# Performance work log

Hardware: AMD Instinct MI355X
Metric: run time of the kernel (lower is better)

## Reference

```python
import jax, jax.numpy as jnp
import numpy as np

N_NODES = 100000
N_EDGES = 1600000
HIDDEN = 128
N_GRAPHS = 64
N_CLASSES = 10


def setup_inputs() -> dict:
    key = jax.random.key(0)
    ks = jax.random.split(key, 10)
    x = jax.random.normal(ks[0], (N_NODES, 1), dtype=jnp.float32)
    edge_index = jax.random.randint(ks[1], (2, N_EDGES), 0, N_NODES, dtype=jnp.int32)
    batch = jnp.sort(jax.random.randint(ks[2], (N_NODES,), 0, N_GRAPHS, dtype=jnp.int32))
    def glorot(k, shape):
        fan_in, fan_out = shape
        s = jnp.sqrt(6.0 / (fan_in + fan_out))
        return jax.random.uniform(k, shape, jnp.float32, -s, s)
    return {
        "x": x,
        "edge_index": edge_index,
        "batch": batch,
        "W1l": glorot(ks[3], (1, HIDDEN)),
        "W1r": glorot(ks[4], (1, HIDDEN)),
        "b1": jnp.zeros((HIDDEN,), jnp.float32),
        "W2l": glorot(ks[5], (HIDDEN, HIDDEN)),
        "W2r": glorot(ks[6], (HIDDEN, HIDDEN)),
        "b2": jnp.zeros((HIDDEN,), jnp.float32),
        "W3l": glorot(ks[7], (HIDDEN, HIDDEN)),
        "W3r": glorot(ks[8], (HIDDEN, HIDDEN)),
        "b3": jnp.zeros((HIDDEN,), jnp.float32),
        "Wfc": glorot(ks[9], (HIDDEN, N_CLASSES)),
        "bfc": jnp.zeros((N_CLASSES,), jnp.float32),
    }


def _sage_conv(x, src, dst, Wl, Wr, b, n_nodes):
    # mean aggregation of source features at destination nodes
    msg = x[src]                                              # [E, d_in]
    agg = jax.ops.segment_sum(msg, dst, num_segments=n_nodes)  # [N, d_in]
    cnt = jax.ops.segment_sum(jnp.ones((src.shape[0], 1), x.dtype), dst,
                              num_segments=n_nodes)            # [N, 1]
    mean = agg / jnp.maximum(cnt, 1.0)
    # PyG SAGEConv: lin_l(mean neighbors) + bias + lin_r(self)
    return mean @ Wl + b + x @ Wr


def reference(x, edge_index, batch, W1l, W1r, b1, W2l, W2r, b2,
              W3l, W3r, b3, Wfc, bfc):
    src, dst = edge_index[0], edge_index[1]
    n = x.shape[0]
    h = jax.nn.relu(_sage_conv(x, src, dst, W1l, W1r, b1, n))
    h = jax.nn.relu(_sage_conv(h, src, dst, W2l, W2r, b2, n))
    h = jax.nn.relu(_sage_conv(h, src, dst, W3l, W3r, b3, n))
    # global_mean_pool over graph ids in `batch`
    pooled = jax.ops.segment_sum(h, batch, num_segments=N_GRAPHS)
    gcnt = jax.ops.segment_sum(jnp.ones((n, 1), h.dtype), batch,
                               num_segments=N_GRAPHS)
    pooled = pooled / jnp.maximum(gcnt, 1.0)
    logits = pooled @ Wfc + bfc
    return jax.nn.log_softmax(logits, axis=1)
```

## Files before the change

### kernel.cpp

```cpp
#include <hip/hip_runtime.h>

typedef unsigned int u32;
typedef unsigned short u16;
typedef short bf16x8 __attribute__((ext_vector_type(8)));
typedef float f32x4 __attribute__((ext_vector_type(4)));
typedef float f32x2 __attribute__((ext_vector_type(2)));
typedef u32 u32x4 __attribute__((ext_vector_type(4)));

#define HBLK 256

__device__ __forceinline__ u16 f2bf(float f) {
  u32 u = __float_as_uint(f);
  u = (u + 0x7FFFu + ((u >> 16) & 1u)) >> 16;
  return (u16)u;
}
__device__ __forceinline__ float bf2f(u32 h) { return __uint_as_float(h << 16); }

__global__ void hist_wprep_kernel(const int* __restrict__ dst, int* __restrict__ boff,
                                  int* __restrict__ btotal, int E, int nbuk, int chunk,
                                  const float* __restrict__ W2l, const float* __restrict__ W2r,
                                  const float* __restrict__ W3l, const float* __restrict__ W3r,
                                  u16* __restrict__ wt2, u16* __restrict__ wt3,
                                  float* __restrict__ pooled, int* __restrict__ gcnt) {
  int idx = blockIdx.x * 256 + threadIdx.x;
  {
    int which = idx >> 15, r = idx & 32767;
    int j = r >> 8, k = r & 255;
    if (which == 0) {
      float v = (k < 128) ? W2l[k * 128 + j] : W2r[(k - 128) * 128 + j];
      wt2[r] = f2bf(v);
    } else {
      float v = (k < 128) ? W3l[k * 128 + j] : W3r[(k - 128) * 128 + j];
      wt3[r] = f2bf(v);
    }
    if (idx < 8192) pooled[idx] = 0.f;
    if (idx < 64) gcnt[idx] = 0;
  }
  __shared__ int h[1024];
  for (int i = threadIdx.x; i < nbuk; i += 256) h[i] = 0;
  __syncthreads();
  int b0 = blockIdx.x * chunk, b1 = min(b0 + chunk, E);
  for (int e = b0 + threadIdx.x; e < b1; e += 256)
    atomicAdd(&h[dst[e] >> 7], 1);
  __syncthreads();
  for (int i = threadIdx.x; i < nbuk; i += 256)
    boff[i * HBLK + blockIdx.x] = atomicAdd(&btotal[i], h[i]);
}

__global__ void scatter2_kernel(const int* __restrict__ src, const int* __restrict__ dst,
                                const int* __restrict__ btotal, const int* __restrict__ boff,
                                u32* __restrict__ part, int* __restrict__ bbase,
                                int E, int nbuk, int chunk) {
  __shared__ int bt[1024];
  __shared__ int wsum[256];
  __shared__ int cur[1024];
  int tid = threadIdx.x;
  int t4 = tid * 4;
  int v0 = (t4 + 0 < nbuk) ? btotal[t4 + 0] : 0;
  int v1 = (t4 + 1 < nbuk) ? btotal[t4 + 1] : 0;
  int v2 = (t4 + 2 < nbuk) ? btotal[t4 + 2] : 0;
  int v3 = (t4 + 3 < nbuk) ? btotal[t4 + 3] : 0;
  int sum = v0 + v1 + v2 + v3;
  wsum[tid] = sum;
  __syncthreads();
  for (int off = 1; off < 256; off <<= 1) {
    int t = (tid >= off) ? wsum[tid - off] : 0;
    __syncthreads();
    wsum[tid] += t;
    __syncthreads();
  }
  int excl = wsum[tid] - sum;
  bt[t4 + 0] = excl;
  bt[t4 + 1] = excl + v0;
  bt[t4 + 2] = excl + v0 + v1;
  bt[t4 + 3] = excl + v0 + v1 + v2;
  __syncthreads();
  for (int i = tid; i < nbuk; i += 256) {
    cur[i] = bt[i] + boff[i * HBLK + blockIdx.x];
    if (blockIdx.x == 0) bbase[i] = bt[i];
  }
  __syncthreads();
  int b0 = blockIdx.x * chunk, b1 = min(b0 + chunk, E);
  for (int e = b0 + tid; e < b1; e += 256) {
    int d = dst[e];
    int pos = atomicAdd(&cur[d >> 7], 1);
    part[pos] = (u32)src[e] | ((u32)(d & 127) << 25);
  }
}

__global__ void scatter3_kernel(const u32* __restrict__ part, const int* __restrict__ bbase,
                                const float* __restrict__ x,
                                const float* __restrict__ W1l, const float* __restrict__ W1r,
                                const float* __restrict__ b1,
                                int* __restrict__ roff, int* __restrict__ csr,
                                u32* __restrict__ h1, int E, int nbuk, int n) {
  int b = blockIdx.x;
  int tid = threadIdx.x;
  int base = bbase[b];
  int end = (b + 1 < nbuk) ? bbase[b + 1] : E;
  __shared__ int cnt[128];
  __shared__ int s[128];
  __shared__ int cur[128];
  __shared__ float xsum[128];
  __shared__ float meanv[128];
  __shared__ float wlA[128], wrA[128], bA[128];
  if (tid < 128) {
    cnt[tid] = 0; xsum[tid] = 0.f;
    wlA[tid] = W1l[tid]; wrA[tid] = W1r[tid]; bA[tid] = b1[tid];
  }
  __syncthreads();
  for (int e = base + tid; e < end; e += 256)
    atomicAdd(&cnt[part[e] >> 25], 1);
  __syncthreads();
  if (tid < 128) s[tid] = cnt[tid];
  __syncthreads();
  for (int off = 1; off < 128; off <<= 1) {
    int t = (tid >= off && tid < 128) ? s[tid - off] : 0;
    __syncthreads();
    if (tid < 128) s[tid] += t;
    __syncthreads();
  }
  if (tid < 128) {
    int excl = s[tid] - cnt[tid];
    cur[tid] = base + excl;
    int node = b * 128 + tid;
    if (node < n) roff[node] = base + excl;
  }
  if (b == 0 && tid == 0) roff[n] = E;
  __syncthreads();
  for (int e = base + tid; e < end; e += 256) {
    u32 p = part[e];
    int sidx = (int)(p & 0x1FFFFFFu);
    int pos = atomicAdd(&cur[p >> 25], 1);
    csr[pos] = sidx;
    atomicAdd(&xsum[p >> 25], x[sidx]);
  }
  __syncthreads();
  if (tid < 128) meanv[tid] = xsum[tid] / (float)max(cnt[tid], 1);
  __syncthreads();
  int nlocal = min(128, n - b * 128);
  for (int q = tid; q < nlocal * 64; q += 256) {
    int ln = q >> 6, w = q & 63;
    int node = b * 128 + ln;
    int j0 = w * 2;
    float m = meanv[ln], xs = x[node];
    float v0 = fmaxf(m * wlA[j0] + xs * wrA[j0] + bA[j0], 0.f);
    float v1 = fmaxf(m * wlA[j0 + 1] + xs * wrA[j0 + 1] + bA[j0 + 1], 0.f);
    h1[(size_t)node * 64 + w] = (u32)f2bf(v0) | ((u32)f2bf(v1) << 16);
  }
}

__global__ void agg_kernel(const int* __restrict__ csr, const int* __restrict__ roff,
                           const u32* __restrict__ hin, u32* __restrict__ outv, int n) {
  int wave = threadIdx.x >> 6, lane = threadIdx.x & 63;
  int i = blockIdx.x * 4 + wave;
  if (i >= n) return;
  int grp = lane >> 4, li = lane & 15;
  int e0 = roff[i], e1 = roff[i + 1];
  f32x2 a[4] = {};
  int e = e0 + grp;
  for (; e + 12 < e1; e += 16) {
    int s0 = csr[e], s1 = csr[e + 4], s2 = csr[e + 8], s3 = csr[e + 12];
    u32x4 v0 = *(const u32x4*)(hin + (size_t)s0 * 64 + li * 4);
    u32x4 v1 = *(const u32x4*)(hin + (size_t)s1 * 64 + li * 4);
    u32x4 v2 = *(const u32x4*)(hin + (size_t)s2 * 64 + li * 4);
    u32x4 v3 = *(const u32x4*)(hin + (size_t)s3 * 64 + li * 4);
#pragma unroll
    for (int w = 0; w < 4; ++w) {
      a[w] += (f32x2){bf2f(v0[w] & 0xFFFFu), bf2f(v0[w] >> 16)};
      a[w] += (f32x2){bf2f(v1[w] & 0xFFFFu), bf2f(v1[w] >> 16)};
      a[w] += (f32x2){bf2f(v2[w] & 0xFFFFu), bf2f(v2[w] >> 16)};
      a[w] += (f32x2){bf2f(v3[w] & 0xFFFFu), bf2f(v3[w] >> 16)};
    }
  }
  for (; e + 4 < e1; e += 8) {
    int s0 = csr[e], s1 = csr[e + 4];
    u32x4 v0 = *(const u32x4*)(hin + (size_t)s0 * 64 + li * 4);
    u32x4 v1 = *(const u32x4*)(hin + (size_t)s1 * 64 + li * 4);
#pragma unroll
    for (int w = 0; w < 4; ++w) {
      a[w] += (f32x2){bf2f(v0[w] & 0xFFFFu), bf2f(v0[w] >> 16)};
      a[w] += (f32x2){bf2f(v1[w] & 0xFFFFu), bf2f(v1[w] >> 16)};
    }
  }
  if (e < e1) {
    int s0 = csr[e];
    u32x4 v0 = *(const u32x4*)(hin + (size_t)s0 * 64 + li * 4);
#pragma unroll
    for (int w = 0; w < 4; ++w)
      a[w] += (f32x2){bf2f(v0[w] & 0xFFFFu), bf2f(v0[w] >> 16)};
  }
#pragma unroll
  for (int w = 0; w < 4; ++w) {
    a[w].x += __shfl_xor(a[w].x, 16, 64);
    a[w].y += __shfl_xor(a[w].y, 16, 64);
    a[w].x += __shfl_xor(a[w].x, 32, 64);
    a[w].y += __shfl_xor(a[w].y, 32, 64);
  }
  if (grp == 0) {
    float inv = 1.f / (float)max(e1 - e0, 1);
    u32x4 o;
#pragma unroll
    for (int w = 0; w < 4; ++w)
      o[w] = (u32)f2bf(a[w].x * inv) | ((u32)f2bf(a[w].y * inv) << 16);
    *(u32x4*)(outv + (size_t)i * 64 + li * 4) = o;
  }
}

__launch_bounds__(1024)
__global__ void mm_kernel(const u16* Aleft, const u16* Aright,
                          const u16* __restrict__ Wt, const float* __restrict__ bias,
                          u16* Out, int n) {
  __shared__ u16 wlds[16384];
  int wave = threadIdx.x >> 6;
  int lane = threadIdx.x & 63;
  int quad = lane >> 4, l16 = lane & 15;
  int row0 = blockIdx.x * 256 + wave * 16;
  int m = row0 + l16;
  int mc = m < n ? m : (n - 1);
  f32x4 acc[8] = {};
  const u16* Ah[2] = {Aleft, Aright};
#pragma unroll
  for (int phase = 0; phase < 2; ++phase) {
    if (phase) __syncthreads();
    for (int c = threadIdx.x; c < 2048; c += 1024) {
      int j = c >> 4, ch = c & 15;
      int swz = ch ^ (j & 15);
      *(u32x4*)(&wlds[j * 128 + swz * 8]) =
          *(const u32x4*)(&Wt[j * 256 + (phase * 16 + ch) * 8]);
    }
    __syncthreads();
    const u16* A = Ah[phase] + (size_t)mc * 128;
#pragma unroll
    for (int s = 0; s < 4; ++s) {
      bf16x8 a = *(const bf16x8*)(A + s * 32 + quad * 8);
      int cc = (s << 2) + quad;
      int swz = cc ^ l16;
#pragma unroll
      for (int t = 0; t < 8; ++t) {
        int j = t * 16 + l16;
        bf16x8 b = *(const bf16x8*)(&wlds[j * 128 + swz * 8]);
        acc[t] = __builtin_amdgcn_mfma_f32_16x16x32_bf16(a, b, acc[t], 0, 0, 0);
      }
    }
  }
#pragma unroll
  for (int t = 0; t < 8; ++t) {
    int j = t * 16 + l16;
    float bj = bias[j];
#pragma unroll
    for (int r = 0; r < 4; ++r) {
      int mr = row0 + quad * 4 + r;
      if (mr < n) {
        float v = acc[t][r] + bj;
        Out[(size_t)mr * 128 + j] = f2bf(fmaxf(v, 0.f));
      }
    }
  }
}

#define PB_NODES 128
__global__ void pool_partial(const int* __restrict__ batch, const u32* __restrict__ h3,
                             float* __restrict__ pooled, int* __restrict__ gcnt, int n) {
  __shared__ int bg[PB_NODES];
  int tid = threadIdx.x;
  int start = blockIdx.x * PB_NODES;
  int cntN = min(PB_NODES, n - start);
  if (tid < cntN) bg[tid] = batch[start + tid];
  __syncthreads();
  int wave = tid >> 6, lane = tid & 63;
  float a0 = 0.f, a1 = 0.f;
  int gcur = -1, cnt = 0;
  int k = wave;
  for (; k + 12 < cntN; k += 16) {
    u32 v0 = h3[(size_t)(start + k) * 64 + lane];
    u32 v1 = h3[(size_t)(start + k + 4) * 64 + lane];
    u32 v2 = h3[(size_t)(start + k + 8) * 64 + lane];
    u32 v3 = h3[(size_t)(start + k + 12) * 64 + lane];
    int g0 = bg[k], g1 = bg[k + 4], g2 = bg[k + 8], g3 = bg[k + 12];
    u32 vv[4] = {v0, v1, v2, v3};
    int gg[4] = {g0, g1, g2, g3};
#pragma unroll
    for (int q = 0; q < 4; ++q) {
      if (gg[q] != gcur) {
        if (gcur >= 0) {
          atomicAdd(&pooled[gcur * 128 + lane * 2], a0);
          atomicAdd(&pooled[gcur * 128 + lane * 2 + 1], a1);
          if (lane == 0) atomicAdd(&gcnt[gcur], cnt);
        }
        gcur = gg[q]; a0 = 0.f; a1 = 0.f; cnt = 0;
      }
      a0 += bf2f(vv[q] & 0xFFFFu);
      a1 += bf2f(vv[q] >> 16);
      cnt++;
    }
  }
  for (; k < cntN; k += 4) {
    u32 v = h3[(size_t)(start + k) * 64 + lane];
    int g = bg[k];
    if (g != gcur) {
      if (gcur >= 0) {
        atomicAdd(&pooled[gcur * 128 + lane * 2], a0);
        atomicAdd(&pooled[gcur * 128 + lane * 2 + 1], a1);
        if (lane == 0) atomicAdd(&gcnt[gcur], cnt);
      }
      gcur = g; a0 = 0.f; a1 = 0.f; cnt = 0;
    }
    a0 += bf2f(v & 0xFFFFu);
    a1 += bf2f(v >> 16);
    cnt++;
  }
  if (gcur >= 0) {
    atomicAdd(&pooled[gcur * 128 + lane * 2], a0);
    atomicAdd(&pooled[gcur * 128 + lane * 2 + 1], a1);
    if (lane == 0) atomicAdd(&gcnt[gcur], cnt);
  }
}

__global__ void head_kernel(const float* __restrict__ pooled, const int* __restrict__ gcnt,
                            const float* __restrict__ Wfc, const float* __restrict__ bfc,
                            float* __restrict__ out) {
  __shared__ float lg[64][10];
  int t = threadIdx.x;
  if (t < 640) {
    int g = t / 10, c = t % 10;
    float inv = 1.f / (float)max(gcnt[g], 1);
    float acc = bfc[c];
    for (int k = 0; k < 128; ++k) acc += pooled[g * 128 + k] * inv * Wfc[k * 10 + c];
    lg[g][c] = acc;
  }
  __syncthreads();
  if (t < 640) {
    int g = t / 10, c = t % 10;
    float mx = -1e30f;
    for (int q = 0; q < 10; ++q) mx = fmaxf(mx, lg[g][q]);
    float se = 0.f;
    for (int q = 0; q < 10; ++q) se += expf(lg[g][q] - mx);
    out[g * 10 + c] = lg[g][c] - mx - logf(se);
  }
}

extern "C" void kernel_launch(void* const* d_in, const int* in_sizes, int n_in,
                              void* d_out, int out_size, void* d_ws, size_t ws_size,
                              hipStream_t stream) {
  const float* x   = (const float*)d_in[0];
  const int* ei    = (const int*)d_in[1];
  const int* batch = (const int*)d_in[2];
  const float* W1l = (const float*)d_in[3];
  const float* W1r = (const float*)d_in[4];
  const float* b1  = (const float*)d_in[5];
  const float* W2l = (const float*)d_in[6];
  const float* W2r = (const float*)d_in[7];
  const float* b2  = (const float*)d_in[8];
  const float* W3l = (const float*)d_in[9];
  const float* W3r = (const float*)d_in[10];
  const float* b3  = (const float*)d_in[11];
  const float* Wfc = (const float*)d_in[12];
  const float* bfc = (const float*)d_in[13];
  float* out = (float*)d_out;
  int N = in_sizes[0];
  int E = in_sizes[1] / 2;
  const int* src = ei;
  const int* dst = ei + E;

  char* p = (char*)d_ws;
  auto alloc = [&](size_t bytes) { void* r = (void*)p; p += (bytes + 255) & ~(size_t)255; return r; };
  int* roff   = (int*)alloc((size_t)(N + 1) * 4);
  int* csr    = (int*)alloc((size_t)E * 4);
  u32* bufA   = (u32*)alloc((size_t)N * 64 * 4);
  u32* bufB   = (u32*)alloc((size_t)N * 64 * 4);
  u16* wt2    = (u16*)alloc(32768 * 2);
  u16* wt3    = (u16*)alloc(32768 * 2);
  float* pooled = (float*)alloc(64 * 128 * 4);
  int* gcnt   = (int*)alloc(64 * 4);
  int* btotal = (int*)alloc(1024 * 4);
  int* bbase  = (int*)alloc(1024 * 4);

  int nbuk = (N + 127) >> 7;
  int* boff = (int*)bufA;
  u32* part = (u32*)bufB;
  int chunk = (E + HBLK - 1) / HBLK;

  hipMemsetAsync(btotal, 0, 1024 * 4, stream);
  hist_wprep_kernel<<<HBLK, 256, 0, stream>>>(dst, boff, btotal, E, nbuk, chunk,
                                              W2l, W2r, W3l, W3r, wt2, wt3,
                                              pooled, gcnt);
  scatter2_kernel<<<HBLK, 256, 0, stream>>>(src, dst, btotal, boff, part, bbase,
                                            E, nbuk, chunk);
  scatter3_kernel<<<nbuk, 256, 0, stream>>>(part, bbase, x, W1l, W1r, b1,
                                            roff, csr, bufA, E, nbuk, N);
  agg_kernel<<<(N + 3) / 4, 256, 0, stream>>>(csr, roff, bufA, bufB, N);
  mm_kernel<<<(N + 255) / 256, 1024, 0, stream>>>((const u16*)bufB, (const u16*)bufA, wt2, b2,
                                                  (u16*)bufB, N);
  agg_kernel<<<(N + 3) / 4, 256, 0, stream>>>(csr, roff, bufB, bufA, N);
  mm_kernel<<<(N + 255) / 256, 1024, 0, stream>>>((const u16*)bufA, (const u16*)bufB, wt3, b3,
                                                  (u16*)bufA, N);
  pool_partial<<<(N + PB_NODES - 1) / PB_NODES, 256, 0, stream>>>(batch, bufA, pooled, gcnt, N);
  head_kernel<<<1, 640, 0, stream>>>(pooled, gcnt, Wfc, bfc, out);
}
```

Measured before the change: 349.3 us.

## Fuse neighbor mean aggregation with SAGE linear layers into one kernel

```diff
diff --git a/kernel.cpp b/kernel.cpp
--- a/kernel.cpp
+++ b/kernel.cpp
@@ -150,14 +150,27 @@
   }
 }
 
-__global__ void agg_kernel(const int* __restrict__ csr, const int* __restrict__ roff,
-                           const u32* __restrict__ hin, u32* __restrict__ outv, int n) {
+__launch_bounds__(1024)
+__global__ void aggmm_kernel(const int* __restrict__ csr, const int* __restrict__ roff,
+                             const u32* __restrict__ hin, const u16* __restrict__ Wt,
+                             const float* __restrict__ bias, u16* __restrict__ out, int n) {
+  __shared__ u16 wlds[16384];
+  __shared__ u16 clds[16 * 136];
   int wave = threadIdx.x >> 6, lane = threadIdx.x & 63;
-  int i = blockIdx.x * 4 + wave;
-  if (i >= n) return;
   int grp = lane >> 4, li = lane & 15;
-  int e0 = roff[i], e1 = roff[i + 1];
+  int quad = grp, l16 = li;
+  int row0 = blockIdx.x * 16;
+  int i = row0 + wave;
+  int c0 = threadIdx.x, c1 = threadIdx.x + 1024;
+  int j0 = c0 >> 4, ch0 = c0 & 15;
+  int j1 = c1 >> 4, ch1 = c1 & 15;
+  u32x4 w0a = *(const u32x4*)(&Wt[j0 * 256 + ch0 * 8]);
+  u32x4 w0b = *(const u32x4*)(&Wt[j1 * 256 + ch1 * 8]);
+  u32x4 w1a = *(const u32x4*)(&Wt[j0 * 256 + (16 + ch0) * 8]);
+  u32x4 w1b = *(const u32x4*)(&Wt[j1 * 256 + (16 + ch1) * 8]);
   f32x2 a[4] = {};
+  int e0 = 0, e1 = 0;
+  if (i < n) { e0 = roff[i]; e1 = roff[i + 1]; }
   int e = e0 + grp;
   for (; e + 12 < e1; e += 16) {
     int s0 = csr[e], s1 = csr[e + 4], s2 = csr[e + 8], s3 = csr[e + 12];
@@ -203,59 +216,56 @@
 #pragma unroll
     for (int w = 0; w < 4; ++w)
       o[w] = (u32)f2bf(a[w].x * inv) | ((u32)f2bf(a[w].y * inv) << 16);
-    *(u32x4*)(outv + (size_t)i * 64 + li * 4) = o;
-  }
-}
-
-__launch_bounds__(1024)
-__global__ void mm_kernel(const u16* Aleft, const u16* Aright,
-                          const u16* __restrict__ Wt, const float* __restrict__ bias,
-                          u16* Out, int n) {
-  __shared__ u16 wlds[16384];
-  int wave = threadIdx.x >> 6;
-  int lane = threadIdx.x & 63;
-  int quad = lane >> 4, l16 = lane & 15;
-  int row0 = blockIdx.x * 256 + wave * 16;
-  int m = row0 + l16;
-  int mc = m < n ? m : (n - 1);
-  f32x4 acc[8] = {};
-  const u16* Ah[2] = {Aleft, Aright};
-#pragma unroll
-  for (int phase = 0; phase < 2; ++phase) {
-    if (phase) __syncthreads();
-    for (int c = threadIdx.x; c < 2048; c += 1024) {
-      int j = c >> 4, ch = c & 15;
-      int swz = ch ^ (j & 15);
-      *(u32x4*)(&wlds[j * 128 + swz * 8]) =
-          *(const u32x4*)(&Wt[j * 256 + (phase * 16 + ch) * 8]);
-    }
-    __syncthreads();
-    const u16* A = Ah[phase] + (size_t)mc * 128;
+    *(u32x4*)(&clds[wave * 136 + li * 8]) = o;
+  }
+  *(u32x4*)(&wlds[j0 * 128 + (ch0 ^ (j0 & 15)) * 8]) = w0a;
+  *(u32x4*)(&wlds[j1 * 128 + (ch1 ^ (j1 & 15)) * 8]) = w0b;
+  __syncthreads();
+  int mm = row0 + l16;
+  int mc = mm < n ? mm : (n - 1);
+  f32x4 acc = {};
+  if (wave < 8) {
 #pragma unroll
     for (int s = 0; s < 4; ++s) {
-      bf16x8 a = *(const bf16x8*)(A + s * 32 + quad * 8);
+      bf16x8 af = *(const bf16x8*)(&clds[l16 * 136 + s * 32 + quad * 8]);
       int cc = (s << 2) + quad;
       int swz = cc ^ l16;
-#pragma unroll
-      for (int t = 0; t < 8; ++t) {
-        int j = t * 16 + l16;
-        bf16x8 b = *(const bf16x8*)(&wlds[j * 128 + swz * 8]);
-        acc[t] = __builtin_amdgcn_mfma_f32_16x16x32_bf16(a, b, acc[t], 0, 0, 0);
-      }
-    }
-  }
-#pragma unroll
-  for (int t = 0; t < 8; ++t) {
-    int j = t * 16 + l16;
+      bf16x8 b = *(const bf16x8*)(&wlds[(wave * 16 + l16) * 128 + swz * 8]);
+      acc = __builtin_amdgcn_mfma_f32_16x16x32_bf16(af, b, acc, 0, 0, 0);
+    }
+  }
+  __syncthreads();
+  *(u32x4*)(&wlds[j0 * 128 + (ch0 ^ (j0 & 15)) * 8]) = w1a;
+  *(u32x4*)(&wlds[j1 * 128 + (ch1 ^ (j1 & 15)) * 8]) = w1b;
+  __syncthreads();
+  if (wave < 8) {
+    const u16* A = (const u16*)hin + (size_t)mc * 128;
+#pragma unroll
+    for (int s = 0; s < 4; ++s) {
+      bf16x8 af = *(const bf16x8*)(A + s * 32 + quad * 8);
+      int cc = (s << 2) + quad;
+      int swz = cc ^ l16;
+      bf16x8 b = *(const bf16x8*)(&wlds[(wave * 16 + l16) * 128 + swz * 8]);
+      acc = __builtin_amdgcn_mfma_f32_16x16x32_bf16(af, b, acc, 0, 0, 0);
+    }
+  }
+  __syncthreads();
+  if (wave < 8) {
+    int j = wave * 16 + l16;
     float bj = bias[j];
 #pragma unroll
     for (int r = 0; r < 4; ++r) {
-      int mr = row0 + quad * 4 + r;
-      if (mr < n) {
-        float v = acc[t][r] + bj;
-        Out[(size_t)mr * 128 + j] = f2bf(fmaxf(v, 0.f));
-      }
-    }
+      float v = acc[r] + bj;
+      clds[(quad * 4 + r) * 136 + j] = f2bf(fmaxf(v, 0.f));
+    }
+  }
+  __syncthreads();
+  if (threadIdx.x < 256) {
+    int rl = threadIdx.x >> 4, ch = threadIdx.x & 15;
+    int mr = row0 + rl;
+    if (mr < n)
+      *(u32x4*)(&out[(size_t)mr * 128 + ch * 8]) =
+          *(const u32x4*)(&clds[rl * 136 + ch * 8]);
   }
 }
 
@@ -389,12 +399,10 @@
                                             E, nbuk, chunk);
   scatter3_kernel<<<nbuk, 256, 0, stream>>>(part, bbase, x, W1l, W1r, b1,
                                             roff, csr, bufA, E, nbuk, N);
-  agg_kernel<<<(N + 3) / 4, 256, 0, stream>>>(csr, roff, bufA, bufB, N);
-  mm_kernel<<<(N + 255) / 256, 1024, 0, stream>>>((const u16*)bufB, (const u16*)bufA, wt2, b2,
-                                                  (u16*)bufB, N);
-  agg_kernel<<<(N + 3) / 4, 256, 0, stream>>>(csr, roff, bufB, bufA, N);
-  mm_kernel<<<(N + 255) / 256, 1024, 0, stream>>>((const u16*)bufA, (const u16*)bufB, wt3, b3,
-                                                  (u16*)bufA, N);
+  aggmm_kernel<<<(N + 15) / 16, 1024, 0, stream>>>(csr, roff, bufA, wt2, b2,
+                                                   (u16*)bufB, N);
+  aggmm_kernel<<<(N + 15) / 16, 1024, 0, stream>>>(csr, roff, bufB, wt3, b3,
+                                                   (u16*)bufA, N);
   pool_partial<<<(N + PB_NODES - 1) / PB_NODES, 256, 0, stream>>>(batch, bufA, pooled, gcnt, N);
   head_kernel<<<1, 640, 0, stream>>>(pooled, gcnt, Wfc, bfc, out);
 }
```

Measured after the change: 471.6 us. 35.0% more time.
